# Optimization experiments

Hardware: AMD Instinct MI355X
Metric: run time of the kernel (lower is better)

The kernel has to match this reference:

```python
import jax, jax.numpy as jnp
import numpy as np

B, L, W, H = 4, 4096, 2048, 8
BW = W // H  # block width


def setup_inputs() -> dict:
    key = jax.random.key(0)
    k = jax.random.split(key, 5)
    std = 1.0 / np.sqrt(BW)  # w_init_variance_scale=1.0
    # a_param init: uniform ring in [0.9,0.999] then inverse-softplus
    u = jax.random.uniform(k[4], (W,), minval=0.9**2 + 1e-8, maxval=0.999**2 + 1e-8)
    a_param = jnp.log(jnp.exp(-0.5 * jnp.log(u)) - 1.0)
    return {
        "x": jax.random.normal(k[0], (B, L, W), dtype=jnp.float32),
        "segment_pos": jnp.arange(L, dtype=jnp.int32),
        "prev_h": jnp.zeros((B, W), dtype=jnp.float32),
        "ig_w": std * jax.random.normal(k[1], (H, BW, BW), dtype=jnp.float32),
        "ig_b": jnp.zeros((H, BW), dtype=jnp.float32),
        "ag_w": std * jax.random.normal(k[2], (H, BW, BW), dtype=jnp.float32),
        "ag_b": jnp.zeros((H, BW), dtype=jnp.float32),
        "a_param": a_param,
    }


@jax.custom_vjp
def sqrt_bound(x):
    return jnp.sqrt(x)

def _sb_fwd(x):
    return jnp.sqrt(x), x

def _sb_bwd(x, g):
    _MAX_SQRT_GRADIENT = 1000.0
    return (g / jnp.sqrt(jnp.clip(4.0 * x, 1.0 / _MAX_SQRT_GRADIENT**2)),)

sqrt_bound.defvjp(_sb_fwd, _sb_bwd)


def block_diag_linear(x, w, b):
    # x: [b,l,(h*i)] -> [b,l,h,i]; w: [h,i,j]; b: [h,j]
    bsz, l, _ = x.shape
    xr = x.reshape(bsz, l, H, BW)
    y = jnp.einsum("blhi,hij->blhj", xr, w) + b
    return y.reshape(bsz, l, W)


def reference(x, segment_pos, prev_h, ig_w, ig_b, ag_w, ag_b, a_param):
    reset = (segment_pos == 0)[None, :, None]  # [1,l,1] bool
    gate_x = jax.nn.sigmoid(block_diag_linear(x, ig_w, ig_b))
    gate_a = jax.nn.sigmoid(block_diag_linear(x, ag_w, ag_b))
    log_a = -8.0 * gate_a * jax.nn.softplus(a_param)  # [b,l,w]
    a = jnp.exp(log_a)
    a_square = jnp.exp(2.0 * log_a)
    gated_x = x * gate_x
    multiplier = sqrt_bound(1.0 - a_square)
    multiplier = jnp.where(reset, 1.0, multiplier)
    normalized_x = gated_x * multiplier.astype(x.dtype)
    a = a * (~reset)  # zero recurrence weight at document boundaries

    # linear scan h_t = a_t * h_{t-1} + x_t, accumulate in float32
    def step(h, inp):
        a_t, x_t = inp
        h = a_t.astype(jnp.float32) * h + x_t.astype(jnp.float32)
        return h, h.astype(x.dtype)

    a_t = jnp.swapaxes(jnp.broadcast_to(a, x.shape), 0, 1)  # [l,b,w]
    x_t = jnp.swapaxes(normalized_x, 0, 1)  # [l,b,w]
    last_h, y = jax.lax.scan(step, prev_h, (a_t, x_t))
    y = jnp.swapaxes(y, 0, 1)  # [b,l,w]
    return y, last_h
```

## Files before the change

### kernel.cpp

```cpp
#include <hip/hip_runtime.h>
#include <hip/hip_bf16.h>
#include <cmath>

#define Bq   4
#define Lq   4096
#define Wq   2048
#define Hq   8
#define Mq   (Bq*Lq)
#define RCH  128
#define NCH  (Lq/RCH)

typedef __bf16 bf16;
typedef __attribute__((ext_vector_type(8))) __bf16 bf16x8;
typedef __attribute__((ext_vector_type(4))) float  f32x4;

#define WS_WT    0
#define WS_C     (2*8*256*256*2)

__global__ __launch_bounds__(256) void prep2(const float* __restrict__ ig_w,
                                             const float* __restrict__ ag_w,
                                             const float* __restrict__ a_param,
                                             bf16* __restrict__ wt, float* __restrict__ c_arr) {
    __shared__ float t[64*65];
    int bid = blockIdx.x;
    int kt = bid & 3, nt = (bid >> 2) & 3, h = (bid >> 4) & 7, g = bid >> 7;
    const float* src = g ? ag_w : ig_w;
    int rr = threadIdx.x >> 6, cc = threadIdx.x & 63;
#pragma unroll
    for (int p = 0; p < 16; p++) {
        int kl = p*4 + rr;
        t[kl*65 + cc] = src[h*65536 + (kt*64 + kl)*256 + nt*64 + cc];
    }
    if (bid < 8) {
        float ap = a_param[bid*256 + threadIdx.x];
        c_arr[bid*256 + threadIdx.x] = 8.0f * log1pf(__expf(ap));
    }
    __syncthreads();
#pragma unroll
    for (int p = 0; p < 16; p++) {
        int nl = p*4 + rr;
        wt[((size_t)((g*8 + h)*256) + nt*64 + nl)*256 + kt*64 + cc] = (bf16)t[cc*65 + nl];
    }
}

__global__ __launch_bounds__(512, 2) void rglru_fused(
    const float* __restrict__ x, const int* __restrict__ segpos,
    const float* __restrict__ prev_h,
    const bf16* __restrict__ wt, const float* __restrict__ igb,
    const float* __restrict__ agb, const float* __restrict__ c_arr,
    float* __restrict__ out)
{
    __shared__ float A_s[RCH*33];
    __shared__ float G_s[RCH*33];
    __shared__ float X_s[RCH*36];
    __shared__ float sgA[512], sgH[512];
    __shared__ float hc[2][32];

    const int tid = threadIdx.x;
    const int bid = blockIdx.x;
    const int h = bid & 7, b = (bid >> 3) & 3, s = bid >> 5;
    const int lane = tid & 63, wv = tid >> 6;
    const int l16 = lane & 15, quad = lane >> 4;
    const int wcol0 = h*256 + s*32;

    bf16x8 wfx[2][8], wfa[2][8];
#pragma unroll
    for (int ct = 0; ct < 2; ct++) {
        const bf16* px = wt + ((size_t)(h*256 + s*32 + ct*16 + l16))*256 + quad*8;
        const bf16* pa = px + (size_t)Hq*256*256;
#pragma unroll
        for (int ks = 0; ks < 8; ks++) {
            wfx[ct][ks] = *(const bf16x8*)(px + (size_t)ks*32);
            wfa[ct][ks] = *(const bf16x8*)(pa + (size_t)ks*32);
        }
    }
    float bxv[2], bav[2], ccv[2];
#pragma unroll
    for (int ct = 0; ct < 2; ct++) {
        int wf = wcol0 + ct*16 + l16;
        bxv[ct] = igb[wf]; bav[ct] = agb[wf]; ccv[ct] = c_arr[wf];
    }
    if (tid < 32) hc[0][tid] = prev_h[b*Wq + wcol0 + tid];

    const float* xrow = x + ((size_t)b*Lq + wv*16 + l16)*Wq + h*256 + quad*8;

    float4 xs[16];
#pragma unroll
    for (int ks = 0; ks < 8; ks++) {
        xs[2*ks]   = *(const float4*)(xrow + ks*32);
        xs[2*ks+1] = *(const float4*)(xrow + ks*32 + 4);
    }

    for (int c = 0; c < NCH; ++c) {
        f32x4 ax[2] = {{0.f,0.f,0.f,0.f},{0.f,0.f,0.f,0.f}};
        f32x4 aa[2] = {{0.f,0.f,0.f,0.f},{0.f,0.f,0.f,0.f}};
#pragma unroll
        for (int ks = 0; ks < 8; ks++) {
            float4 u0 = xs[2*ks], u1 = xs[2*ks+1];
            if (ks == s) {
                float* xp = &X_s[(wv*16 + l16)*36 + quad*8];
                *(float4*)xp = u0; *(float4*)(xp + 4) = u1;
            }
            bf16x8 af;
            af[0]=(bf16)u0.x; af[1]=(bf16)u0.y; af[2]=(bf16)u0.z; af[3]=(bf16)u0.w;
            af[4]=(bf16)u1.x; af[5]=(bf16)u1.y; af[6]=(bf16)u1.z; af[7]=(bf16)u1.w;
            ax[0] = __builtin_amdgcn_mfma_f32_16x16x32_bf16(af, wfx[0][ks], ax[0], 0,0,0);
            ax[1] = __builtin_amdgcn_mfma_f32_16x16x32_bf16(af, wfx[1][ks], ax[1], 0,0,0);
            aa[0] = __builtin_amdgcn_mfma_f32_16x16x32_bf16(af, wfa[0][ks], aa[0], 0,0,0);
            aa[1] = __builtin_amdgcn_mfma_f32_16x16x32_bf16(af, wfa[1][ks], aa[1], 0,0,0);
        }

        {
            const float* xn_ = xrow + (size_t)((c < NCH-1) ? c+1 : c)*RCH*Wq;
#pragma unroll
            for (int ks = 0; ks < 8; ks++) {
                xs[2*ks]   = *(const float4*)(xn_ + ks*32);
                xs[2*ks+1] = *(const float4*)(xn_ + ks*32 + 4);
            }
        }

#pragma unroll
        for (int r = 0; r < 4; r++) {
            int grow = wv*16 + quad*4 + r;
            bool rst = (segpos[c*RCH + grow] == 0);
#pragma unroll
            for (int ct = 0; ct < 2; ct++) {
                float zx = ax[ct][r] + bxv[ct];
                float za = aa[ct][r] + bav[ct];
                float gx = __builtin_amdgcn_rcpf(1.f + __expf(-zx));
                float ga = __builtin_amdgcn_rcpf(1.f + __expf(-za));
                float av = __expf(-ga * ccv[ct]);
                float mult = __builtin_amdgcn_sqrtf(fmaf(-av, av, 1.f));
                if (rst) { av = 0.f; mult = 1.f; }
                A_s[grow*33 + ct*16 + l16] = av;
                G_s[grow*33 + ct*16 + l16] = gx * mult;
            }
        }
        __syncthreads();

        const int col2 = tid & 31, seg = tid >> 5;
        float Pl[8], hl[8];
        float A = 1.f, hv = 0.f;
#pragma unroll
        for (int r = 0; r < 8; r++) {
            int grow = seg*8 + r;
            float a  = A_s[grow*33 + col2];
            float xn = G_s[grow*33 + col2] * X_s[grow*36 + col2];
            hv = fmaf(a, hv, xn); A *= a;
            Pl[r] = A; hl[r] = hv;
        }
        sgA[tid] = A; sgH[tid] = hv;
        __syncthreads();

        float h0 = hc[c & 1][col2];
#pragma unroll
        for (int sp = 0; sp < 15; sp++)
            if (sp < seg) h0 = fmaf(sgA[sp*32 + col2], h0, sgH[sp*32 + col2]);

        float* yp = out + ((size_t)b*Lq + c*RCH + seg*8)*Wq + wcol0 + col2;
#pragma unroll
        for (int r = 0; r < 8; r++)
            yp[(size_t)r*Wq] = fmaf(Pl[r], h0, hl[r]);

        if (seg == 15) hc[(c+1) & 1][col2] = fmaf(Pl[7], h0, hl[7]);
    }
    __syncthreads();
    if (tid < 32) out[(size_t)Mq*Wq + b*Wq + wcol0 + tid] = hc[NCH & 1][tid];
}

extern "C" void kernel_launch(void* const* d_in, const int* in_sizes, int n_in,
                              void* d_out, int out_size, void* d_ws, size_t ws_size,
                              hipStream_t stream) {
    const float* x       = (const float*)d_in[0];
    const int*   segpos  = (const int*)  d_in[1];
    const float* prev_h  = (const float*)d_in[2];
    const float* ig_w    = (const float*)d_in[3];
    const float* ig_b    = (const float*)d_in[4];
    const float* ag_w    = (const float*)d_in[5];
    const float* ag_b    = (const float*)d_in[6];
    const float* a_param = (const float*)d_in[7];
    float* out = (float*)d_out;

    char* ws = (char*)d_ws;
    bf16*   wt    = (bf16*)  (ws + WS_WT);
    float*  c_arr = (float*) (ws + WS_C);

    prep2<<<256, 256, 0, stream>>>(ig_w, ag_w, a_param, wt, c_arr);
    rglru_fused<<<256, 512, 0, stream>>>(x, segpos, prev_h, wt, ig_b, ag_b, c_arr, out);
}
```

Baseline: 451.4 us.

## Scan directly on MFMA accumulator layout with shuffles, weights in LDS

The chunked linear scan now runs on the MFMA output fragments in registers. It does a per-lane serial scan over 4 rows, then a cross-quad shuffle scan inside the wavefront, then a cross-wave carry through small LDS arrays. This removes the A/G/X shared-memory staging and one of the two block barriers per chunk. The gate x values and segment positions are prefetched per chunk in the accumulator layout. Weights move from registers into LDS and occupancy drops to 1 block per CU, which frees registers but adds LDS reads on every MFMA step.

```diff
diff --git a/kernel.cpp b/kernel.cpp
--- a/kernel.cpp
+++ b/kernel.cpp
@@ -43,17 +43,15 @@
     }
 }
 
-__global__ __launch_bounds__(512, 2) void rglru_fused(
+__global__ __launch_bounds__(512, 1) void rglru_fused(
     const float* __restrict__ x, const int* __restrict__ segpos,
     const float* __restrict__ prev_h,
     const bf16* __restrict__ wt, const float* __restrict__ igb,
     const float* __restrict__ agb, const float* __restrict__ c_arr,
     float* __restrict__ out)
 {
-    __shared__ float A_s[RCH*33];
-    __shared__ float G_s[RCH*33];
-    __shared__ float X_s[RCH*36];
-    __shared__ float sgA[512], sgH[512];
+    __shared__ bf16x8 Wl[32*64];
+    __shared__ float sgA[2][8][32], sgH[2][8][32];
     __shared__ float hc[2][32];
 
     const int tid = threadIdx.x;
@@ -63,16 +61,11 @@
     const int l16 = lane & 15, quad = lane >> 4;
     const int wcol0 = h*256 + s*32;
 
-    bf16x8 wfx[2][8], wfa[2][8];
-#pragma unroll
-    for (int ct = 0; ct < 2; ct++) {
-        const bf16* px = wt + ((size_t)(h*256 + s*32 + ct*16 + l16))*256 + quad*8;
-        const bf16* pa = px + (size_t)Hq*256*256;
-#pragma unroll
-        for (int ks = 0; ks < 8; ks++) {
-            wfx[ct][ks] = *(const bf16x8*)(px + (size_t)ks*32);
-            wfa[ct][ks] = *(const bf16x8*)(pa + (size_t)ks*32);
-        }
+    for (int t = tid; t < 2048; t += 512) {
+        int ln = t & 63, ks = (t >> 6) & 7, ct = (t >> 9) & 1, g = t >> 10;
+        int n  = s*32 + ct*16 + (ln & 15);
+        int k  = ks*32 + (ln >> 4)*8;
+        Wl[t] = *(const bf16x8*)&wt[((size_t)((g*8 + h)*256 + n))*256 + k];
     }
     float bxv[2], bav[2], ccv[2];
 #pragma unroll
@@ -82,87 +75,125 @@
     }
     if (tid < 32) hc[0][tid] = prev_h[b*Wq + wcol0 + tid];
 
-    const float* xrow = x + ((size_t)b*Lq + wv*16 + l16)*Wq + h*256 + quad*8;
-
-    float4 xs[16];
+    const float* xfrag = x + ((size_t)b*Lq + wv*16 + l16)*Wq + h*256 + quad*8;
+    const float* xgate = x + ((size_t)b*Lq + wv*16 + quad*4)*Wq + wcol0 + l16;
+    const int*   spp   = segpos + wv*16 + quad*4;
+
+    float4 xs[16]; float xg[8]; int sp[4];
 #pragma unroll
     for (int ks = 0; ks < 8; ks++) {
-        xs[2*ks]   = *(const float4*)(xrow + ks*32);
-        xs[2*ks+1] = *(const float4*)(xrow + ks*32 + 4);
-    }
+        xs[2*ks]   = *(const float4*)(xfrag + ks*32);
+        xs[2*ks+1] = *(const float4*)(xfrag + ks*32 + 4);
+    }
+#pragma unroll
+    for (int r = 0; r < 4; r++) {
+        sp[r] = spp[r];
+#pragma unroll
+        for (int ct = 0; ct < 2; ct++)
+            xg[r*2+ct] = xgate[(size_t)r*Wq + ct*16];
+    }
+    __syncthreads();
 
     for (int c = 0; c < NCH; ++c) {
-        f32x4 ax[2] = {{0.f,0.f,0.f,0.f},{0.f,0.f,0.f,0.f}};
-        f32x4 aa[2] = {{0.f,0.f,0.f,0.f},{0.f,0.f,0.f,0.f}};
+        const int cur = c & 1, nxt = cur ^ 1;
+        const int cn  = (c < NCH-1) ? c+1 : c;
+
+        f32x4 ax[2], aa[2];
+#pragma unroll
+        for (int j = 0; j < 2; j++) { ax[j] = (f32x4){0.f,0.f,0.f,0.f}; aa[j] = (f32x4){0.f,0.f,0.f,0.f}; }
 #pragma unroll
         for (int ks = 0; ks < 8; ks++) {
             float4 u0 = xs[2*ks], u1 = xs[2*ks+1];
-            if (ks == s) {
-                float* xp = &X_s[(wv*16 + l16)*36 + quad*8];
-                *(float4*)xp = u0; *(float4*)(xp + 4) = u1;
-            }
             bf16x8 af;
             af[0]=(bf16)u0.x; af[1]=(bf16)u0.y; af[2]=(bf16)u0.z; af[3]=(bf16)u0.w;
             af[4]=(bf16)u1.x; af[5]=(bf16)u1.y; af[6]=(bf16)u1.z; af[7]=(bf16)u1.w;
-            ax[0] = __builtin_amdgcn_mfma_f32_16x16x32_bf16(af, wfx[0][ks], ax[0], 0,0,0);
-            ax[1] = __builtin_amdgcn_mfma_f32_16x16x32_bf16(af, wfx[1][ks], ax[1], 0,0,0);
-            aa[0] = __builtin_amdgcn_mfma_f32_16x16x32_bf16(af, wfa[0][ks], aa[0], 0,0,0);
-            aa[1] = __builtin_amdgcn_mfma_f32_16x16x32_bf16(af, wfa[1][ks], aa[1], 0,0,0);
-        }
-
+            bf16x8 w0 = Wl[(0*8+ks)*64 + lane];
+            bf16x8 w1 = Wl[(1*8+ks)*64 + lane];
+            bf16x8 w2 = Wl[(2*8+ks)*64 + lane];
+            bf16x8 w3 = Wl[(3*8+ks)*64 + lane];
+            ax[0] = __builtin_amdgcn_mfma_f32_16x16x32_bf16(af, w0, ax[0], 0,0,0);
+            ax[1] = __builtin_amdgcn_mfma_f32_16x16x32_bf16(af, w1, ax[1], 0,0,0);
+            aa[0] = __builtin_amdgcn_mfma_f32_16x16x32_bf16(af, w2, aa[0], 0,0,0);
+            aa[1] = __builtin_amdgcn_mfma_f32_16x16x32_bf16(af, w3, aa[1], 0,0,0);
+        }
         {
-            const float* xn_ = xrow + (size_t)((c < NCH-1) ? c+1 : c)*RCH*Wq;
+            const float* xp = xfrag + (size_t)cn*RCH*Wq;
 #pragma unroll
             for (int ks = 0; ks < 8; ks++) {
-                xs[2*ks]   = *(const float4*)(xn_ + ks*32);
-                xs[2*ks+1] = *(const float4*)(xn_ + ks*32 + 4);
-            }
-        }
-
+                xs[2*ks]   = *(const float4*)(xp + ks*32);
+                xs[2*ks+1] = *(const float4*)(xp + ks*32 + 4);
+            }
+        }
+
+        float av[8], xn[8];
 #pragma unroll
         for (int r = 0; r < 4; r++) {
-            int grow = wv*16 + quad*4 + r;
-            bool rst = (segpos[c*RCH + grow] == 0);
+            bool rst = (sp[r] == 0);
 #pragma unroll
             for (int ct = 0; ct < 2; ct++) {
                 float zx = ax[ct][r] + bxv[ct];
                 float za = aa[ct][r] + bav[ct];
                 float gx = __builtin_amdgcn_rcpf(1.f + __expf(-zx));
                 float ga = __builtin_amdgcn_rcpf(1.f + __expf(-za));
-                float av = __expf(-ga * ccv[ct]);
-                float mult = __builtin_amdgcn_sqrtf(fmaf(-av, av, 1.f));
-                if (rst) { av = 0.f; mult = 1.f; }
-                A_s[grow*33 + ct*16 + l16] = av;
-                G_s[grow*33 + ct*16 + l16] = gx * mult;
-            }
+                float a  = __expf(-ga * ccv[ct]);
+                float mult = __builtin_amdgcn_sqrtf(fmaf(-a, a, 1.f));
+                if (rst) { a = 0.f; mult = 1.f; }
+                av[r*2+ct] = a;
+                xn[r*2+ct] = gx * mult * xg[r*2+ct];
+            }
+        }
+        {
+            const float* xp = xgate + (size_t)cn*RCH*Wq;
+#pragma unroll
+            for (int r = 0; r < 4; r++) {
+                sp[r] = spp[cn*RCH + r];
+#pragma unroll
+                for (int ct = 0; ct < 2; ct++)
+                    xg[r*2+ct] = xp[(size_t)r*Wq + ct*16];
+            }
+        }
+
+        float Pl[8], hl[8], Awv[2], Hwv[2];
+#pragma unroll
+        for (int ct = 0; ct < 2; ct++) {
+            float A = 1.f, hv = 0.f;
+#pragma unroll
+            for (int r = 0; r < 4; r++) {
+                hv = fmaf(av[r*2+ct], hv, xn[r*2+ct]);
+                A *= av[r*2+ct];
+                Pl[ct*4+r] = A; hl[ct*4+r] = hv;
+            }
+            float Asc = A, Hsc = hv;
+            float Apv = __shfl(Asc, (lane-16) & 63), Hpv = __shfl(Hsc, (lane-16) & 63);
+            if (quad >= 1) { Hsc = fmaf(Asc, Hpv, Hsc); Asc *= Apv; }
+            Apv = __shfl(Asc, (lane-32) & 63); Hpv = __shfl(Hsc, (lane-32) & 63);
+            if (quad >= 2) { Hsc = fmaf(Asc, Hpv, Hsc); Asc *= Apv; }
+            float Aex = __shfl(Asc, (lane-16) & 63), Hex = __shfl(Hsc, (lane-16) & 63);
+            if (quad == 0) { Aex = 1.f; Hex = 0.f; }
+#pragma unroll
+            for (int r = 0; r < 4; r++) {
+                hl[ct*4+r] = fmaf(Pl[ct*4+r], Hex, hl[ct*4+r]);
+                Pl[ct*4+r] *= Aex;
+            }
+            Awv[ct] = Asc; Hwv[ct] = Hsc;
+            if (quad == 3) { sgA[cur][wv][ct*16+l16] = Asc; sgH[cur][wv][ct*16+l16] = Hsc; }
         }
         __syncthreads();
 
-        const int col2 = tid & 31, seg = tid >> 5;
-        float Pl[8], hl[8];
-        float A = 1.f, hv = 0.f;
-#pragma unroll
-        for (int r = 0; r < 8; r++) {
-            int grow = seg*8 + r;
-            float a  = A_s[grow*33 + col2];
-            float xn = G_s[grow*33 + col2] * X_s[grow*36 + col2];
-            hv = fmaf(a, hv, xn); A *= a;
-            Pl[r] = A; hl[r] = hv;
-        }
-        sgA[tid] = A; sgH[tid] = hv;
-        __syncthreads();
-
-        float h0 = hc[c & 1][col2];
-#pragma unroll
-        for (int sp = 0; sp < 15; sp++)
-            if (sp < seg) h0 = fmaf(sgA[sp*32 + col2], h0, sgH[sp*32 + col2]);
-
-        float* yp = out + ((size_t)b*Lq + c*RCH + seg*8)*Wq + wcol0 + col2;
-#pragma unroll
-        for (int r = 0; r < 8; r++)
-            yp[(size_t)r*Wq] = fmaf(Pl[r], h0, hl[r]);
-
-        if (seg == 15) hc[(c+1) & 1][col2] = fmaf(Pl[7], h0, hl[7]);
+#pragma unroll
+        for (int ct = 0; ct < 2; ct++) {
+            int col = ct*16 + l16;
+            float h0 = hc[cur][col];
+#pragma unroll
+            for (int w = 0; w < 7; w++)
+                if (w < wv) h0 = fmaf(sgA[cur][w][col], h0, sgH[cur][w][col]);
+            float* yp = out + ((size_t)b*Lq + (size_t)c*RCH + wv*16 + quad*4)*Wq + wcol0 + col;
+#pragma unroll
+            for (int r = 0; r < 4; r++)
+                yp[(size_t)r*Wq] = fmaf(Pl[ct*4+r], h0, hl[ct*4+r]);
+            if (wv == 7 && quad == 3)
+                hc[nxt][col] = fmaf(Awv[ct], h0, Hwv[ct]);
+        }
     }
     __syncthreads();
     if (tid < 32) out[(size_t)Mq*Wq + b*Wq + wcol0 + tid] = hc[NCH & 1][tid];
```

Result: faster. 366.5 us (-18.8%).
